# Performance work log

Hardware: AMD Instinct MI355X
Metric: run time of the kernel (lower is better)

## Reference

```python
import jax, jax.numpy as jnp
import numpy as np


def _ccl(x, w, b):
    # FFT-domain circular conv: rfft2 -> complex multiply + sum over c_in -> irfft2 + bias
    H, W = x.shape[-2], x.shape[-1]
    xf = jnp.fft.rfft2(x)                 # [B, Ci, H, Wf] complex
    wf = jnp.fft.rfft2(w, s=(H, W))       # [Co, Ci, H, Wf] complex
    hf = jnp.einsum('bihw,oihw->bohw', xf, wf)
    return jnp.fft.irfft2(hf, s=(H, W)) + b[:, None, None]


def _maxpool(x, ph, pw):
    B, C, H, W = x.shape
    return x.reshape(B, C, H // ph, ph, W // pw, pw).max(axis=(3, 5))


def _upsample_zero(x, sh, sw):
    B, C, H, W = x.shape
    y = jnp.zeros((B, C, H * sh, W * sw), dtype=x.dtype)
    return y.at[:, :, ::sh, ::sw].set(x)


def setup_inputs() -> dict:
    key = jax.random.key(0)
    ks = jax.random.split(key, 11)
    inp = {"x": jax.random.normal(ks[0], (16, 2, 64, 256), dtype=jnp.float32)}
    specs = [  # (c_out, c_in, kh, kw)
        (50, 1, 3, 7), (50, 50, 3, 7), (50, 50, 3, 5), (50, 50, 3, 7), (1, 50, 3, 7)]
    for i, (co, ci, kh, kw) in enumerate(specs):
        K = float(np.sqrt(1.0 / (ci * kh * kw)))
        inp[f"w{i+1}"] = (2 * jax.random.uniform(ks[2 * i + 1], (co, ci, kh, kw), dtype=jnp.float32) - 1) * K
        inp[f"b{i+1}"] = (2 * jax.random.uniform(ks[2 * i + 2], (co,), dtype=jnp.float32) - 1) * K
    return inp


def reference(x, w1, b1, w2, b2, w3, b3, w4, b4, w5, b5):
    H, W = x.shape[-2], x.shape[-1]
    h = x.reshape(-1, 1, H, W)                       # [2B, 1, 64, 256]
    h = jax.nn.relu(_maxpool(_ccl(h, w1, b1), 2, 4))  # [2B, 50, 32, 64]
    h = jax.nn.relu(_maxpool(_ccl(h, w2, b2), 2, 4))  # [2B, 50, 16, 16]
    h = h.reshape(-1, 2, h.shape[-3], h.shape[-2], h.shape[-1])
    h = h[:, 0] + h[:, 1].mean(axis=(-1, -2))[..., None, None]  # [B, 50, 16, 16]
    h = jax.nn.relu(_ccl(_upsample_zero(h, 2, 4), w3, b3))       # [B, 50, 32, 64]
    h = jax.nn.relu(_ccl(_upsample_zero(h, 2, 4), w4, b4))       # [B, 50, 64, 256]
    h = jax.nn.sigmoid(_ccl(h, w5, b5))                          # [B, 1, 64, 256]
    return h.squeeze(1)
```

## Files before the change

kernel.cpp:

```cpp
#include <hip/hip_runtime.h>
#include <math.h>

__global__ __launch_bounds__(256) void k1(const float* __restrict__ x,
                                          const float* __restrict__ w1,
                                          const float* __restrict__ b1,
                                          float* __restrict__ a1,
                                          const float* __restrict__ w2,
                                          const float* __restrict__ w3,
                                          const float* __restrict__ w4,
                                          float* __restrict__ w2t,
                                          float* __restrict__ w3t,
                                          float* __restrict__ w4t) {
  int b = blockIdx.z;
  int pr0 = blockIdx.x * 4;
  int co0 = blockIdx.y * 10;
  int ty = threadIdx.x >> 6;
  int pc = threadIdx.x & 63;
  int pr = pr0 + ty;
  const float* xb = x + b * (64 * 256);
  float xw[4][10];
#pragma unroll
  for (int r = 0; r < 4; ++r) {
    int row = (2 * pr - 2 + r) & 63;
#pragma unroll
    for (int c = 0; c < 10; ++c) {
      int col = (4 * pc - 6 + c) & 255;
      xw[r][c] = xb[row * 256 + col];
    }
  }
#pragma unroll
  for (int cq = 0; cq < 10; ++cq) {
    int co = co0 + cq;
    const float* wp = w1 + co * 21;
    float m = -1e30f;
#pragma unroll
    for (int iy = 0; iy < 2; ++iy) {
#pragma unroll
      for (int jx = 0; jx < 4; ++jx) {
        float s = 0.f;
#pragma unroll
        for (int di = 0; di < 3; ++di)
#pragma unroll
          for (int dj = 0; dj < 7; ++dj)
            s = fmaf(xw[iy + 2 - di][jx + 6 - dj], wp[di * 7 + dj], s);
        m = fmaxf(m, s);
      }
    }
    float v = fmaxf(m + b1[co], 0.f);
    a1[((b * 50 + co) * 32 + pr) * 64 + pc] = v;
  }
  if (blockIdx.y == 0) {
    int base = (blockIdx.z * 8 + blockIdx.x) * 256 + threadIdx.x;
    for (int i = base; i < 90000; i += 65536) {
      if (i < 52500) {
        int co = i % 50, r = i / 50;
        w2t[i] = w2[co * 1050 + r];
        w4t[i] = w4[co * 1050 + r];
      } else {
        int j2 = i - 52500;
        int co = j2 % 50, r = j2 / 50;
        w3t[j2] = w3[co * 750 + r];
      }
    }
  }
}

__global__ __launch_bounds__(256) void k2(const float* __restrict__ a1,
                                          const float* __restrict__ w2t,
                                          const float* __restrict__ b2,
                                          float* __restrict__ a2) {
  __shared__ __align__(16) float sm[3840];
  int b = blockIdx.z;
  int r0 = blockIdx.x * 4;
  int co0 = blockIdx.y * 10;
  int y = threadIdx.x >> 6;
  int xcol = threadIdx.x & 63;
  const float* p[7];
#pragma unroll
  for (int dj = 0; dj < 7; ++dj) p[dj] = sm + y * 64 + ((xcol - dj) & 63);
  float acc[10];
#pragma unroll
  for (int co = 0; co < 10; ++co) acc[co] = b2[co0 + co];
  const float* ain = a1 + b * (50 * 2048);
  for (int cci = 0; cci < 5; ++cci) {
    __syncthreads();
    for (int e = threadIdx.x; e < 960; e += 256) {
      int ci = e / 96;
      int rem = e - ci * 96;
      int rr = rem >> 4;
      int c4 = rem & 15;
      int row = (r0 - 2 + rr) & 31;
      *(float4*)&sm[(ci * 6 + rr) * 64 + c4 * 4] =
          *(const float4*)&ain[(cci * 10 + ci) * 2048 + row * 64 + c4 * 4];
    }
    __syncthreads();
    const float* q0 = p[0]; const float* q1 = p[1]; const float* q2 = p[2];
    const float* q3 = p[3]; const float* q4 = p[4]; const float* q5 = p[5];
    const float* q6 = p[6];
    for (int ci = 0; ci < 10; ++ci) {
      const float* wci = w2t + (cci * 10 + ci) * 1050 + co0;
#pragma unroll
      for (int di = 0; di < 3; ++di) {
        const int ro = (2 - di) * 64;
        float xv0 = q0[ro], xv1 = q1[ro], xv2 = q2[ro], xv3 = q3[ro];
        float xv4 = q4[ro], xv5 = q5[ro], xv6 = q6[ro];
        const float* wr = wci + di * 7 * 50;
#pragma unroll
        for (int co = 0; co < 10; ++co) acc[co] = fmaf(xv0, wr[co], acc[co]);
#pragma unroll
        for (int co = 0; co < 10; ++co) acc[co] = fmaf(xv1, wr[50 + co], acc[co]);
#pragma unroll
        for (int co = 0; co < 10; ++co) acc[co] = fmaf(xv2, wr[100 + co], acc[co]);
#pragma unroll
        for (int co = 0; co < 10; ++co) acc[co] = fmaf(xv3, wr[150 + co], acc[co]);
#pragma unroll
        for (int co = 0; co < 10; ++co) acc[co] = fmaf(xv4, wr[200 + co], acc[co]);
#pragma unroll
        for (int co = 0; co < 10; ++co) acc[co] = fmaf(xv5, wr[250 + co], acc[co]);
#pragma unroll
        for (int co = 0; co < 10; ++co) acc[co] = fmaf(xv6, wr[300 + co], acc[co]);
      }
      q0 += 384; q1 += 384; q2 += 384; q3 += 384; q4 += 384; q5 += 384; q6 += 384;
    }
  }
  __syncthreads();
#pragma unroll
  for (int k = 0; k < 10; ++k)
    sm[k * 256 + y * 64 + xcol] = acc[k];
  __syncthreads();
  for (int w = threadIdx.x; w < 320; w += 256) {
    int cop = w / 32;
    int pr = (w >> 4) & 1;
    int pc = w & 15;
    float m = -1e30f;
#pragma unroll
    for (int yy = 0; yy < 2; ++yy)
#pragma unroll
      for (int xx = 0; xx < 4; ++xx)
        m = fmaxf(m, sm[cop * 256 + (pr * 2 + yy) * 64 + pc * 4 + xx]);
    m = fmaxf(m, 0.f);
    a2[((b * 50 + co0 + cop) * 16 + (r0 >> 1) + pr) * 16 + pc] = m;
  }
}

__global__ __launch_bounds__(512) void k3(const float* __restrict__ a2,
                                          const float* __restrict__ w3t,
                                          const float* __restrict__ b3,
                                          float* __restrict__ a3) {
  __shared__ float ts[4000];
  __shared__ float mean_s[64];
  __shared__ float part[200];
  int b = blockIdx.z;
  int r0 = blockIdx.x * 8;
  int co0 = blockIdx.y * 10;
  int tid = threadIdx.x;
  const float* aodd = a2 + (2 * b + 1) * (50 * 256);
  if (tid < 200) {
    int ci = tid >> 2, p = tid & 3;
    float s = 0.f;
    for (int k = 0; k < 64; ++k) s += aodd[ci * 256 + p * 64 + k];
    part[tid] = s;
  }
  __syncthreads();
  if (tid < 50)
    mean_s[tid] = (part[4 * tid] + part[4 * tid + 1] + part[4 * tid + 2] + part[4 * tid + 3]) * (1.f / 256.f);
  __syncthreads();
  const float* aev = a2 + (2 * b) * (50 * 256);
  for (int e = tid; e < 4000; e += 512) {
    int ci = e / 80;
    int rr = (e >> 4) % 5;
    int tc = e & 15;
    int trow = ((r0 >> 1) - 1 + rr) & 15;
    ts[e] = aev[ci * 256 + trow * 16 + tc] + mean_s[ci];
  }
  __syncthreads();
  int wv = __builtin_amdgcn_readfirstlane(tid >> 6);
  int lane = tid & 63;
  int p = wv >> 2;
  int m = wv & 3;
  int q = lane & 15;
  int yidx = lane >> 4;
  int i = r0 + 2 * yidx + p;
  int j = 4 * q + m;
  float acc[10];
#pragma unroll
  for (int co = 0; co < 10; ++co) acc[co] = b3[co0 + co];
  int ndi = (p == 0) ? 2 : 1;
  int ndj = (m == 0) ? 2 : 1;
  for (int aa = 0; aa < ndi; ++aa) {
    int di = (p == 0) ? (2 * aa) : 1;
    int rr = 1 + ((2 * yidx + p - di) >> 1);
    for (int e2 = 0; e2 < ndj; ++e2) {
      int dj = (m == 0) ? (4 * e2) : m;
      int tc = ((j - dj + 64) >> 2) & 15;
      for (int ci = 0; ci < 50; ++ci) {
        float xv = ts[ci * 80 + rr * 16 + tc];
        const float* wrow = w3t + (ci * 15 + di * 5 + dj) * 50 + co0;
#pragma unroll
        for (int co = 0; co < 10; ++co)
          acc[co] = fmaf(xv, wrow[co], acc[co]);
      }
    }
  }
  float* aout = a3 + b * (50 * 2048);
#pragma unroll
  for (int co = 0; co < 10; ++co)
    aout[(co0 + co) * 2048 + i * 64 + j] = fmaxf(acc[co], 0.f);
}

__global__ __launch_bounds__(512) void k4(const float* __restrict__ a3,
                                          const float* __restrict__ w4t,
                                          const float* __restrict__ b4,
                                          float* __restrict__ a4) {
  __shared__ __align__(16) float s4[9600];
  int b = blockIdx.z;
  int r0 = blockIdx.x * 4;
  int co0 = blockIdx.y * 10;
  int tid = threadIdx.x;
  const float* ain = a3 + b * (50 * 2048);
  int prb = (r0 >> 1) - 1;
  for (int e = tid; e < 2400; e += 512) {
    int ci = e / 48;
    int rem = e - ci * 48;
    int rr = rem >> 4;
    int c4 = rem & 15;
    int row = (prb + rr) & 31;
    *(float4*)&s4[(ci * 3 + rr) * 64 + c4 * 4] =
        *(const float4*)&ain[ci * 2048 + row * 64 + c4 * 4];
  }
  __syncthreads();
  int wv = __builtin_amdgcn_readfirstlane(tid >> 6);
  int lane = tid & 63;
  int rowsel = wv >> 2;
  int m = wv & 3;
  int j = 4 * lane + m;
  float acc[2][10];
#pragma unroll
  for (int co = 0; co < 10; ++co) {
    float bc = b4[co0 + co];
    acc[0][co] = bc; acc[1][co] = bc;
  }
  int ndi = (rowsel == 0) ? 2 : 1;
  int ndj = (m < 3) ? 2 : 1;
  for (int aa = 0; aa < ndi; ++aa) {
    int di = (rowsel == 0) ? (2 * aa) : 1;
    int rrb = 1 + ((rowsel - di) >> 1);
    for (int e2 = 0; e2 < ndj; ++e2) {
      int dj = m + 4 * e2;
      int tc = ((j - dj) >> 2) & 63;
      for (int ci = 0; ci < 50; ++ci) {
        float xv0 = s4[ci * 192 + rrb * 64 + tc];
        float xv1 = s4[ci * 192 + (rrb + 1) * 64 + tc];
        const float* wrow = w4t + (ci * 21 + di * 7 + dj) * 50 + co0;
#pragma unroll
        for (int co = 0; co < 10; ++co) {
          float w = wrow[co];
          acc[0][co] = fmaf(xv0, w, acc[0][co]);
          acc[1][co] = fmaf(xv1, w, acc[1][co]);
        }
      }
    }
  }
  float* aout = a4 + b * (50 * 16384);
  int i0 = r0 + rowsel, i1 = r0 + rowsel + 2;
#pragma unroll
  for (int co = 0; co < 10; ++co) {
    aout[(co0 + co) * 16384 + i0 * 256 + j] = fmaxf(acc[0][co], 0.f);
    aout[(co0 + co) * 16384 + i1 * 256 + j] = fmaxf(acc[1][co], 0.f);
  }
}

__global__ __launch_bounds__(512) void k5(const float* __restrict__ a4,
                                          const float* __restrict__ w5,
                                          const float* __restrict__ b5,
                                          float* __restrict__ out) {
  __shared__ __align__(16) float s5[4000];
  __shared__ float smw5[1056];
  int bid = blockIdx.x;
  int b = bid >> 5;
  int rem = bid & 31;
  int r0 = (rem >> 2) * 8;
  int jb = (rem & 3) * 64;
  int tid = threadIdx.x;
  int y = tid >> 6;
  int q = tid & 63;
  for (int e = tid; e < 1050; e += 512) smw5[e] = w5[e];
  float acc = b5[0];
  const float* ain = a4 + b * (50 * 16384);
  for (int cc = 0; cc < 10; ++cc) {
    __syncthreads();
    for (int e = tid; e < 1000; e += 512) {
      int ci = e / 200;
      int rem2 = e - ci * 200;
      int rr = rem2 / 20;
      int g = rem2 - rr * 20;
      int row = (r0 - 2 + rr) & 63;
      int col = (jb + 4 * g - 8) & 255;
      *(float4*)&s5[(ci * 10 + rr) * 80 + 4 * g] =
          *(const float4*)&ain[(cc * 5 + ci) * 16384 + row * 256 + col];
    }
    __syncthreads();
#pragma unroll
    for (int ci = 0; ci < 5; ++ci) {
#pragma unroll
      for (int di = 0; di < 3; ++di) {
        const float* base = s5 + ci * 800 + (y + 2 - di) * 80 + 8 + q;
        const float* wp = smw5 + ((cc * 5 + ci) * 3 + di) * 7;
#pragma unroll
        for (int dj = 0; dj < 7; ++dj)
          acc = fmaf(base[-dj], wp[dj], acc);
      }
    }
  }
  out[b * 16384 + (r0 + y) * 256 + jb + q] = 1.f / (1.f + expf(-acc));
}

extern "C" void kernel_launch(void* const* d_in, const int* in_sizes, int n_in,
                              void* d_out, int out_size, void* d_ws, size_t ws_size,
                              hipStream_t stream) {
  (void)in_sizes; (void)n_in; (void)out_size; (void)ws_size;
  const float* x  = (const float*)d_in[0];
  const float* w1 = (const float*)d_in[1];
  const float* b1 = (const float*)d_in[2];
  const float* w2 = (const float*)d_in[3];
  const float* b2 = (const float*)d_in[4];
  const float* w3 = (const float*)d_in[5];
  const float* b3 = (const float*)d_in[6];
  const float* w4 = (const float*)d_in[7];
  const float* b4 = (const float*)d_in[8];
  const float* w5 = (const float*)d_in[9];
  const float* b5 = (const float*)d_in[10];
  float* out = (float*)d_out;
  float* ws  = (float*)d_ws;
  float* w2t = ws;
  float* w3t = w2t + 52500;
  float* w4t = w3t + 37500;
  float* a1  = w4t + 52500;
  float* a2  = a1 + 32 * 50 * 32 * 64;
  float* a3  = a2 + 32 * 50 * 16 * 16;
  float* a4  = a3 + 16 * 50 * 32 * 64;
  hipLaunchKernelGGL(k1, dim3(8, 5, 32), dim3(256), 0, stream, x, w1, b1, a1,
                     w2, w3, w4, w2t, w3t, w4t);
  hipLaunchKernelGGL(k2, dim3(8, 5, 32), dim3(256), 0, stream, a1, w2t, b2, a2);
  hipLaunchKernelGGL(k3, dim3(4, 5, 16), dim3(512), 0, stream, a2, w3t, b3, a3);
  hipLaunchKernelGGL(k4, dim3(16, 5, 16), dim3(512), 0, stream, a3, w4t, b4, a4);
  hipLaunchKernelGGL(k5, dim3(512), dim3(512), 0, stream, a4, w5, b5, out);
}
```

Baseline: 313.3 us.

## Compute two output rows per thread in k2 to reuse weights

Each k2 thread now computes two adjacent conv output rows, the vertical pair of the 2x4 maxpool window, with two accumulator sets. Each weight load feeds two FMAs, the vertical max is taken in registers, and the block tile grows from 4 to 8 rows, halving the grid. This cuts weight loads and halo reloads per output, at the cost of more registers, more shared memory and fewer blocks in flight.

```diff
diff --git a/kernel.cpp b/kernel.cpp
--- a/kernel.cpp
+++ b/kernel.cpp
@@ -69,28 +69,31 @@
                                           const float* __restrict__ w2t,
                                           const float* __restrict__ b2,
                                           float* __restrict__ a2) {
-  __shared__ __align__(16) float sm[3840];
+  __shared__ __align__(16) float sm[6400];
   int b = blockIdx.z;
-  int r0 = blockIdx.x * 4;
+  int r0 = blockIdx.x * 8;
   int co0 = blockIdx.y * 10;
   int y = threadIdx.x >> 6;
   int xcol = threadIdx.x & 63;
   const float* p[7];
 #pragma unroll
-  for (int dj = 0; dj < 7; ++dj) p[dj] = sm + y * 64 + ((xcol - dj) & 63);
-  float acc[10];
-#pragma unroll
-  for (int co = 0; co < 10; ++co) acc[co] = b2[co0 + co];
+  for (int dj = 0; dj < 7; ++dj) p[dj] = sm + 2 * y * 64 + ((xcol - dj) & 63);
+  float accA[10], accB[10];
+#pragma unroll
+  for (int co = 0; co < 10; ++co) {
+    float bc = b2[co0 + co];
+    accA[co] = bc; accB[co] = bc;
+  }
   const float* ain = a1 + b * (50 * 2048);
   for (int cci = 0; cci < 5; ++cci) {
     __syncthreads();
-    for (int e = threadIdx.x; e < 960; e += 256) {
-      int ci = e / 96;
-      int rem = e - ci * 96;
+    for (int e = threadIdx.x; e < 1600; e += 256) {
+      int ci = e / 160;
+      int rem = e - ci * 160;
       int rr = rem >> 4;
       int c4 = rem & 15;
       int row = (r0 - 2 + rr) & 31;
-      *(float4*)&sm[(ci * 6 + rr) * 64 + c4 * 4] =
+      *(float4*)&sm[(ci * 10 + rr) * 64 + c4 * 4] =
           *(const float4*)&ain[(cci * 10 + ci) * 2048 + row * 64 + c4 * 4];
     }
     __syncthreads();
@@ -101,43 +104,66 @@
       const float* wci = w2t + (cci * 10 + ci) * 1050 + co0;
 #pragma unroll
       for (int di = 0; di < 3; ++di) {
-        const int ro = (2 - di) * 64;
-        float xv0 = q0[ro], xv1 = q1[ro], xv2 = q2[ro], xv3 = q3[ro];
-        float xv4 = q4[ro], xv5 = q5[ro], xv6 = q6[ro];
-        const float* wr = wci + di * 7 * 50;
-#pragma unroll
-        for (int co = 0; co < 10; ++co) acc[co] = fmaf(xv0, wr[co], acc[co]);
-#pragma unroll
-        for (int co = 0; co < 10; ++co) acc[co] = fmaf(xv1, wr[50 + co], acc[co]);
-#pragma unroll
-        for (int co = 0; co < 10; ++co) acc[co] = fmaf(xv2, wr[100 + co], acc[co]);
-#pragma unroll
-        for (int co = 0; co < 10; ++co) acc[co] = fmaf(xv3, wr[150 + co], acc[co]);
-#pragma unroll
-        for (int co = 0; co < 10; ++co) acc[co] = fmaf(xv4, wr[200 + co], acc[co]);
-#pragma unroll
-        for (int co = 0; co < 10; ++co) acc[co] = fmaf(xv5, wr[250 + co], acc[co]);
-#pragma unroll
-        for (int co = 0; co < 10; ++co) acc[co] = fmaf(xv6, wr[300 + co], acc[co]);
-      }
-      q0 += 384; q1 += 384; q2 += 384; q3 += 384; q4 += 384; q5 += 384; q6 += 384;
+        const int roA = (2 - di) * 64;
+        const int roB = (3 - di) * 64;
+        float xa0 = q0[roA], xa1 = q1[roA], xa2 = q2[roA], xa3 = q3[roA];
+        float xa4 = q4[roA], xa5 = q5[roA], xa6 = q6[roA];
+        float xb0 = q0[roB], xb1 = q1[roB], xb2 = q2[roB], xb3 = q3[roB];
+        float xb4 = q4[roB], xb5 = q5[roB], xb6 = q6[roB];
+        const float* wr = wci + di * 350;
+#pragma unroll
+        for (int co = 0; co < 10; ++co) {
+          float w = wr[co];
+          accA[co] = fmaf(xa0, w, accA[co]); accB[co] = fmaf(xb0, w, accB[co]);
+        }
+#pragma unroll
+        for (int co = 0; co < 10; ++co) {
+          float w = wr[50 + co];
+          accA[co] = fmaf(xa1, w, accA[co]); accB[co] = fmaf(xb1, w, accB[co]);
+        }
+#pragma unroll
+        for (int co = 0; co < 10; ++co) {
+          float w = wr[100 + co];
+          accA[co] = fmaf(xa2, w, accA[co]); accB[co] = fmaf(xb2, w, accB[co]);
+        }
+#pragma unroll
+        for (int co = 0; co < 10; ++co) {
+          float w = wr[150 + co];
+          accA[co] = fmaf(xa3, w, accA[co]); accB[co] = fmaf(xb3, w, accB[co]);
+        }
+#pragma unroll
+        for (int co = 0; co < 10; ++co) {
+          float w = wr[200 + co];
+          accA[co] = fmaf(xa4, w, accA[co]); accB[co] = fmaf(xb4, w, accB[co]);
+        }
+#pragma unroll
+        for (int co = 0; co < 10; ++co) {
+          float w = wr[250 + co];
+          accA[co] = fmaf(xa5, w, accA[co]); accB[co] = fmaf(xb5, w, accB[co]);
+        }
+#pragma unroll
+        for (int co = 0; co < 10; ++co) {
+          float w = wr[300 + co];
+          accA[co] = fmaf(xa6, w, accA[co]); accB[co] = fmaf(xb6, w, accB[co]);
+        }
+      }
+      q0 += 640; q1 += 640; q2 += 640; q3 += 640; q4 += 640; q5 += 640; q6 += 640;
     }
   }
   __syncthreads();
 #pragma unroll
   for (int k = 0; k < 10; ++k)
-    sm[k * 256 + y * 64 + xcol] = acc[k];
-  __syncthreads();
-  for (int w = threadIdx.x; w < 320; w += 256) {
-    int cop = w / 32;
-    int pr = (w >> 4) & 1;
-    int pc = w & 15;
+    sm[k * 256 + y * 64 + xcol] = fmaxf(accA[k], accB[k]);
+  __syncthreads();
+  for (int w = threadIdx.x; w < 640; w += 256) {
+    int cop = w >> 6;
+    int rem = w & 63;
+    int pr = rem >> 4;
+    int pc = rem & 15;
     float m = -1e30f;
 #pragma unroll
-    for (int yy = 0; yy < 2; ++yy)
-#pragma unroll
-      for (int xx = 0; xx < 4; ++xx)
-        m = fmaxf(m, sm[cop * 256 + (pr * 2 + yy) * 64 + pc * 4 + xx]);
+    for (int xx = 0; xx < 4; ++xx)
+      m = fmaxf(m, sm[cop * 256 + pr * 64 + pc * 4 + xx]);
     m = fmaxf(m, 0.f);
     a2[((b * 50 + co0 + cop) * 16 + (r0 >> 1) + pr) * 16 + pc] = m;
   }
@@ -341,7 +367,7 @@
   float* a4  = a3 + 16 * 50 * 32 * 64;
   hipLaunchKernelGGL(k1, dim3(8, 5, 32), dim3(256), 0, stream, x, w1, b1, a1,
                      w2, w3, w4, w2t, w3t, w4t);
-  hipLaunchKernelGGL(k2, dim3(8, 5, 32), dim3(256), 0, stream, a1, w2t, b2, a2);
+  hipLaunchKernelGGL(k2, dim3(4, 5, 32), dim3(256), 0, stream, a1, w2t, b2, a2);
   hipLaunchKernelGGL(k3, dim3(4, 5, 16), dim3(512), 0, stream, a2, w3t, b3, a3);
   hipLaunchKernelGGL(k4, dim3(16, 5, 16), dim3(512), 0, stream, a3, w4t, b4, a4);
   hipLaunchKernelGGL(k5, dim3(512), dim3(512), 0, stream, a4, w5, b5, out);
```

After: 329.0 us. 1.05x slower.
